# Optimization experiments

Hardware: AMD Instinct MI355X
Metric: run time of the kernel (lower is better)

Reference implementation:

```python
import jax, jax.numpy as jnp
import numpy as np

N, E = 10000, 320000
IN_DIM, OUT_DIM, HEADS = 256, 32, 8
HD = OUT_DIM * HEADS  # 256
EPS = 1e-16  # PyG softmax epsilon


def _make_conv_params(key, in_dim, heads, d):
    hd = heads * d
    ks = jax.random.split(key, 8)
    s = 0.02
    return {
        'Wq': jax.random.normal(ks[0], (in_dim, hd)) * s,
        'bq': jnp.zeros((hd,)),
        'Wk': jax.random.normal(ks[1], (in_dim, hd)) * s,
        'bk': jnp.zeros((hd,)),
        'Wv': jax.random.normal(ks[2], (in_dim, hd)) * s,
        'bv': jnp.zeros((hd,)),
        'We': jax.random.normal(ks[3], (1, hd)) * s,          # lin_edge, no bias
        'Wskip': jax.random.normal(ks[4], (in_dim, hd)) * s,  # lin_skip
        'bskip': jnp.zeros((hd,)),
        'Wbeta': jax.random.normal(ks[5], (3 * hd, 1)) * s,   # lin_beta, no bias
    }


def transformer_conv(x, src, dst, edge_attr, p, heads, d):
    # x: [N, F]; edge_attr: [E, 1]
    n = x.shape[0]
    q = (x @ p['Wq'] + p['bq']).reshape(n, heads, d)
    k = (x @ p['Wk'] + p['bk']).reshape(n, heads, d)
    v = (x @ p['Wv'] + p['bv']).reshape(n, heads, d)
    e = (edge_attr @ p['We']).reshape(-1, heads, d)  # [E, H, D]
    kj = k[src] + e                                  # [E, H, D]
    vj = v[src] + e
    # per-edge attention logits
    alpha = jnp.einsum('ehd,ehd->eh', q[dst], kj) / jnp.sqrt(jnp.asarray(d, x.dtype))
    # segment softmax over incoming edges of each dst node
    m = jax.ops.segment_max(alpha, dst, num_segments=n)     # [N, H]
    m = jnp.where(jnp.isfinite(m), m, 0.0)
    ex = jnp.exp(alpha - m[dst])
    denom = jax.ops.segment_sum(ex, dst, num_segments=n)    # [N, H]
    w = ex / (denom[dst] + EPS)                              # [E, H]
    out = jax.ops.segment_sum(w[:, :, None] * vj, dst, num_segments=n)  # [N, H, D]
    out = out.reshape(n, heads * d)
    # beta-gated skip connection
    xr = x @ p['Wskip'] + p['bskip']
    beta = jax.nn.sigmoid(jnp.concatenate([out, xr, out - xr], axis=-1) @ p['Wbeta'])  # [N, 1]
    return beta * xr + (1.0 - beta) * out


def setup_inputs() -> dict:
    key = jax.random.key(0)
    kx, ke, kw, k1, k2 = jax.random.split(key, 5)
    inp = {
        'x': jax.random.normal(kx, (N, IN_DIM), dtype=jnp.float32),
        'edge_index': jax.random.randint(ke, (2, E), 0, N, dtype=jnp.int64),
        'edge_weight': jax.random.uniform(kw, (E,), dtype=jnp.float32),
    }
    p1 = _make_conv_params(k1, IN_DIM, HEADS, OUT_DIM)
    p2 = _make_conv_params(k2, HD, HEADS, OUT_DIM)
    for name, v in p1.items():
        inp[name + '1'] = v
    for name, v in p2.items():
        inp[name + '2'] = v
    return inp


def reference(x, edge_index, edge_weight,
              Wq1, bq1, Wk1, bk1, Wv1, bv1, We1, Wskip1, bskip1, Wbeta1,
              Wq2, bq2, Wk2, bk2, Wv2, bv2, We2, Wskip2, bskip2, Wbeta2):
    src, dst = edge_index[0], edge_index[1]
    ea = edge_weight[:, None]  # [E, 1]
    p1 = dict(Wq=Wq1, bq=bq1, Wk=Wk1, bk=bk1, Wv=Wv1, bv=bv1, We=We1,
              Wskip=Wskip1, bskip=bskip1, Wbeta=Wbeta1)
    p2 = dict(Wq=Wq2, bq=bq2, Wk=Wk2, bk=bk2, Wv=Wv2, bv=bv2, We=We2,
              Wskip=Wskip2, bskip=bskip2, Wbeta=Wbeta2)
    h = transformer_conv(x, src, dst, ea, p1, HEADS, OUT_DIM)
    h = transformer_conv(h, src, dst, ea, p2, HEADS, OUT_DIM)
    h = transformer_conv(h, src, dst, ea, p2, HEADS, OUT_DIM)  # conv2 applied twice, shared weights
    return h
```

## Files before the change

### kernel.cpp

```cpp
#include <hip/hip_runtime.h>
#include <hip/hip_bf16.h>
#include <math.h>

#define NN 10000
#define EE 320000
#define DIM 256
#define NROWS 10016
#define SCANB 40

typedef __attribute__((ext_vector_type(8))) _Float16 f16x8;
typedef __attribute__((ext_vector_type(4))) _Float16 f16x4;
typedef __attribute__((ext_vector_type(4))) float f32x4;

__device__ __forceinline__ float bf2f(unsigned short u) {
  union { unsigned int ui; float f; } cv;
  cv.ui = ((unsigned int)u) << 16;
  return cv.f;
}

__global__ void k_detect(const unsigned int* __restrict__ xw, const int* __restrict__ ei,
                         int* __restrict__ flags) {
  int lane = threadIdx.x;
  int wild = 0;
  for (int t = 0; t < 16; ++t) {
    unsigned int w = xw[t * 64 + lane];
    unsigned int lo = w & 0xffffu;
    float f = bf2f((unsigned short)lo);
    float af = fabsf(f);
    if (lo != 0u && (af > 1e4f || af < 1e-30f)) wild++;
  }
  #pragma unroll
  for (int m = 1; m < 64; m <<= 1) wild += __shfl_xor(wild, m);
  int zeros = 0;
  for (int t = 0; t < 2; ++t) {
    if (ei[(t * 64 + lane) * 2 + 1] == 0) zeros++;
  }
  #pragma unroll
  for (int m = 1; m < 64; m <<= 1) zeros += __shfl_xor(zeros, m);
  if (lane == 0) {
    flags[0] = (wild > 100) ? 1 : 0;
    flags[1] = (zeros > 100) ? 1 : 0;
  }
}

struct PBatch { const void* src[20]; int off[21]; };

__global__ void k_cvt_params(PBatch b, float* __restrict__ out, const int* __restrict__ flags) {
  int isf = flags[0];
  int total = b.off[20];
  for (int i = blockIdx.x * blockDim.x + threadIdx.x; i < total; i += gridDim.x * blockDim.x) {
    int k = 0;
    while (i >= b.off[k + 1]) k++;
    int j = i - b.off[k];
    out[i] = isf ? ((const float*)b.src[k])[j] : bf2f(((const unsigned short*)b.src[k])[j]);
  }
}

__global__ void k_split_x(const void* __restrict__ in, _Float16* __restrict__ Ah,
                          _Float16* __restrict__ Al, const int* __restrict__ flags) {
  int isf = flags[0];
  int i = blockIdx.x * blockDim.x + threadIdx.x;
  if (i >= NROWS * DIM / 4) return;
  f16x4 h, l;
  if (i >= NN * DIM / 4) {
    h = (f16x4)(_Float16)0.f;
    l = (f16x4)(_Float16)0.f;
  } else {
    float v[4];
    if (isf) {
      float4 t = reinterpret_cast<const float4*>(in)[i];
      v[0] = t.x; v[1] = t.y; v[2] = t.z; v[3] = t.w;
    } else {
      ushort4 t = reinterpret_cast<const ushort4*>(in)[i];
      v[0] = bf2f(t.x); v[1] = bf2f(t.y); v[2] = bf2f(t.z); v[3] = bf2f(t.w);
    }
    #pragma unroll
    for (int j = 0; j < 4; ++j) {
      _Float16 hh = (_Float16)v[j];
      h[j] = hh;
      l[j] = (_Float16)(v[j] - (float)hh);
    }
  }
  reinterpret_cast<f16x4*>(Ah)[i] = h;
  reinterpret_cast<f16x4*>(Al)[i] = l;
}

struct WPtrs { const float* W[8]; };

__global__ void k_split_w(WPtrs wp, _Float16* __restrict__ Bh) {
  int i = blockIdx.x * blockDim.x + threadIdx.x;
  if (i >= 8 * 65536) return;
  int m = i >> 16;
  int col = (i >> 8) & 255;
  int k = i & 255;
  Bh[i] = (_Float16)wp.W[m][k * 256 + col];
}

struct BPtrs { const float* B[8]; };

__global__ void k_bias(BPtrs bp, float* __restrict__ bvec) {
  int i = blockIdx.x * blockDim.x + threadIdx.x;
  if (i >= 2048) return;
  int m = i >> 8;
  bvec[i] = bp.B[m][i & 255];
}

__global__ void k_idx_count(const int* __restrict__ ei, int* __restrict__ s32,
                            int* __restrict__ d32, int* __restrict__ counts,
                            const int* __restrict__ flags) {
  int i64 = flags[1];
  int i = blockIdx.x * blockDim.x + threadIdx.x;
  if (i < EE) {
    int s, d;
    if (i64) { s = ei[2 * i]; d = ei[2 * (EE + i)]; }
    else     { s = ei[i];     d = ei[EE + i]; }
    s32[i] = s; d32[i] = d;
    atomicAdd(&counts[d], 1);
  }
}

__global__ __launch_bounds__(256) void k_scan1(const int* __restrict__ counts,
                                               int* __restrict__ tmpoff,
                                               int* __restrict__ bsum) {
  __shared__ int s[256];
  int t = threadIdx.x;
  int i = blockIdx.x * 256 + t;
  int v = (i < NN) ? counts[i] : 0;
  s[t] = v;
  __syncthreads();
  for (int off = 1; off < 256; off <<= 1) {
    int x = (t >= off) ? s[t - off] : 0;
    __syncthreads();
    s[t] += x;
    __syncthreads();
  }
  if (i < NN) tmpoff[i] = s[t] - v;
  if (t == 255) bsum[blockIdx.x] = s[255];
}

__global__ void k_scan2(const int* __restrict__ bsum, int* __restrict__ bbase) {
  int lane = threadIdx.x;
  int v = (lane < SCANB) ? bsum[lane] : 0;
  int incl = v;
  #pragma unroll
  for (int off = 1; off < 64; off <<= 1) {
    int t = __shfl_up(incl, off);
    if (lane >= off) incl += t;
  }
  if (lane < SCANB) bbase[lane] = incl - v;
}

__global__ __launch_bounds__(256) void k_scan3(const int* __restrict__ tmpoff,
                                               const int* __restrict__ bbase,
                                               int* __restrict__ offsets,
                                               int* __restrict__ cursor) {
  int i = blockIdx.x * 256 + threadIdx.x;
  if (i < NN) {
    int o = tmpoff[i] + bbase[i >> 8];
    offsets[i] = o;
    cursor[i] = o;
  }
  if (i == 0) offsets[NN] = EE;
}

__global__ void k_fill_sort(const int* __restrict__ d32, const int* __restrict__ s32,
                            const void* __restrict__ ew, int* __restrict__ cursor,
                            int* __restrict__ srcS, float* __restrict__ wS,
                            const int* __restrict__ flags) {
  int isf = flags[0];
  int i = blockIdx.x * blockDim.x + threadIdx.x;
  if (i < EE) {
    float wv = isf ? ((const float*)ew)[i] : bf2f(((const unsigned short*)ew)[i]);
    int p = atomicAdd(&cursor[d32[i]], 1);
    srcS[p] = s32[i];
    wS[p] = wv;
  }
}

__global__ __launch_bounds__(256, 4) void k_gemm_mfma(
    const _Float16* __restrict__ Ah, const _Float16* __restrict__ Al,
    const _Float16* __restrict__ Bh, const float* __restrict__ bvec,
    float* __restrict__ Qf, _Float16* __restrict__ KVh, float* __restrict__ XRf) {
  int tid = (int)threadIdx.x;
  int wave = tid >> 6, lane = tid & 63;
  int lr = lane & 15;
  int kg = (lane >> 4) << 3;
  int mat = blockIdx.y;
  int rowBase = blockIdx.x << 5;
  int colBase = (mat << 8) + (wave << 6);
  const _Float16* a0 = Ah + (size_t)(rowBase + lr) * 256 + kg;
  const _Float16* a1 = Al + (size_t)(rowBase + lr) * 256 + kg;
  const _Float16* b0 = Bh + (size_t)(colBase + lr) * 256 + kg;
  f32x4 acc[2][4] = {};
  #pragma unroll
  for (int ks = 0; ks < 256; ks += 32) {
    f16x8 ah0 = *reinterpret_cast<const f16x8*>(a0 + ks);
    f16x8 ah1 = *reinterpret_cast<const f16x8*>(a0 + 16 * 256 + ks);
    f16x8 bh[4];
    #pragma unroll
    for (int cf = 0; cf < 4; ++cf)
      bh[cf] = *reinterpret_cast<const f16x8*>(b0 + cf * 16 * 256 + ks);
    #pragma unroll
    for (int cf = 0; cf < 4; ++cf) {
      acc[0][cf] = __builtin_amdgcn_mfma_f32_16x16x32_f16(ah0, bh[cf], acc[0][cf], 0, 0, 0);
      acc[1][cf] = __builtin_amdgcn_mfma_f32_16x16x32_f16(ah1, bh[cf], acc[1][cf], 0, 0, 0);
    }
    if (mat == 3) {
      f16x8 al0 = *reinterpret_cast<const f16x8*>(a1 + ks);
      f16x8 al1 = *reinterpret_cast<const f16x8*>(a1 + 16 * 256 + ks);
      #pragma unroll
      for (int cf = 0; cf < 4; ++cf) {
        acc[0][cf] = __builtin_amdgcn_mfma_f32_16x16x32_f16(al0, bh[cf], acc[0][cf], 0, 0, 0);
        acc[1][cf] = __builtin_amdgcn_mfma_f32_16x16x32_f16(al1, bh[cf], acc[1][cf], 0, 0, 0);
      }
    }
  }
  int rj = (lane >> 4) << 2;
  int colLoc = (wave << 6);
  #pragma unroll
  for (int rf = 0; rf < 2; ++rf) {
    #pragma unroll
    for (int cf = 0; cf < 4; ++cf) {
      int col = colLoc + cf * 16 + lr;
      float bb = bvec[(mat << 8) + col];
      #pragma unroll
      for (int j = 0; j < 4; ++j) {
        int row = rowBase + rf * 16 + rj + j;
        if (row < NN) {
          float val = acc[rf][cf][j] + bb;
          if (mat == 0)      Qf[(size_t)row * DIM + col] = val;
          else if (mat == 3) XRf[(size_t)row * DIM + col] = val;
          else KVh[(size_t)row * 512 + ((mat == 2) ? 256 : 0) + col] = (_Float16)val;
        }
      }
    }
  }
}

#define ATT_STEP(KK, VV, WW) do { \
    float part = q4.x * fmaf(WW, we4.x, (float)KK[0]) + q4.y * fmaf(WW, we4.y, (float)KK[1]) \
               + q4.z * fmaf(WW, we4.z, (float)KK[2]) + q4.w * fmaf(WW, we4.w, (float)KK[3]); \
    part += __shfl_xor(part, 1); \
    part += __shfl_xor(part, 2); \
    part += __shfl_xor(part, 4); \
    float alpha = part * 0.17677669529663687f; \
    float nm = fmaxf(m, alpha); \
    float sc = __expf(m - nm); \
    float pe = __expf(alpha - nm); \
    l = l * sc + pe; \
    a0 = fmaf(a0, sc, pe * fmaf(WW, we4.x, (float)VV[0])); \
    a1 = fmaf(a1, sc, pe * fmaf(WW, we4.y, (float)VV[1])); \
    a2 = fmaf(a2, sc, pe * fmaf(WW, we4.z, (float)VV[2])); \
    a3 = fmaf(a3, sc, pe * fmaf(WW, we4.w, (float)VV[3])); \
    m = nm; \
  } while (0)

__global__ __launch_bounds__(256) void k_attn(
    const float* __restrict__ Qf, const _Float16* __restrict__ KVh,
    const float* __restrict__ XRf, const float* __restrict__ We,
    const float* __restrict__ Wb, const int* __restrict__ srcS,
    const float* __restrict__ wS, const int* __restrict__ offsets,
    _Float16* __restrict__ Ah, _Float16* __restrict__ Al,
    float* __restrict__ FinalOut) {
  int wid = (int)threadIdx.x >> 6, lane = (int)threadIdx.x & 63;
  int node = blockIdx.x * 4 + wid;
  if (node >= NN) return;
  int d0 = lane * 4;
  const float4 q4 = *reinterpret_cast<const float4*>(&Qf[(size_t)node * DIM + d0]);
  const float4 x4 = *reinterpret_cast<const float4*>(&XRf[(size_t)node * DIM + d0]);
  const float4 we4 = *reinterpret_cast<const float4*>(&We[d0]);
  const float4 wo = *reinterpret_cast<const float4*>(&Wb[d0]);
  const float4 wx = *reinterpret_cast<const float4*>(&Wb[DIM + d0]);
  const float4 wd = *reinterpret_cast<const float4*>(&Wb[2 * DIM + d0]);
  int beg = offsets[node], end = offsets[node + 1];
  beg = __builtin_amdgcn_readfirstlane(beg);
  end = __builtin_amdgcn_readfirstlane(end);
  float m = -INFINITY, l = 0.f, a0 = 0.f, a1 = 0.f, a2 = 0.f, a3 = 0.f;
  if (end > beg) {
    int pLast = end - 1;
    int sA = srcS[beg];
    float wA = wS[beg];
    int p1 = (beg + 1 <= pLast) ? beg + 1 : pLast;
    int sB = srcS[p1];
    float wB = wS[p1];
    const _Float16* rA = KVh + (size_t)sA * 512 + d0;
    const _Float16* rB = KVh + (size_t)sB * 512 + d0;
    f16x4 kA = *reinterpret_cast<const f16x4*>(rA);
    f16x4 vA = *reinterpret_cast<const f16x4*>(rA + 256);
    f16x4 kB = *reinterpret_cast<const f16x4*>(rB);
    f16x4 vB = *reinterpret_cast<const f16x4*>(rB + 256);
    int p = beg;
    #pragma unroll 2
    for (; p + 2 < end; ++p) {
      int sN = srcS[p + 2];
      float wN = wS[p + 2];
      const _Float16* rN = KVh + (size_t)sN * 512 + d0;
      f16x4 kN = *reinterpret_cast<const f16x4*>(rN);
      f16x4 vN = *reinterpret_cast<const f16x4*>(rN + 256);
      ATT_STEP(kA, vA, wA);
      kA = kB; vA = vB; wA = wB;
      kB = kN; vB = vN; wB = wN;
    }
    ATT_STEP(kA, vA, wA);
    if (p + 1 < end) ATT_STEP(kB, vB, wB);
  }
  float inv = 1.f / (l + 1e-16f);
  float o0 = a0 * inv, o1 = a1 * inv, o2 = a2 * inv, o3 = a3 * inv;
  float part = o0 * wo.x + o1 * wo.y + o2 * wo.z + o3 * wo.w
             + x4.x * wx.x + x4.y * wx.y + x4.z * wx.z + x4.w * wx.w
             + (o0 - x4.x) * wd.x + (o1 - x4.y) * wd.y
             + (o2 - x4.z) * wd.z + (o3 - x4.w) * wd.w;
  #pragma unroll
  for (int msk = 1; msk < 64; msk <<= 1) part += __shfl_xor(part, msk);
  float beta = 1.f / (1.f + __expf(-part));
  float h0 = beta * x4.x + (1.f - beta) * o0;
  float h1 = beta * x4.y + (1.f - beta) * o1;
  float h2 = beta * x4.z + (1.f - beta) * o2;
  float h3 = beta * x4.w + (1.f - beta) * o3;
  if (FinalOut) {
    float4 h; h.x = h0; h.y = h1; h.z = h2; h.w = h3;
    *reinterpret_cast<float4*>(&FinalOut[(size_t)node * DIM + d0]) = h;
  } else {
    f16x4 hh, ll;
    _Float16 t0 = (_Float16)h0, t1 = (_Float16)h1, t2 = (_Float16)h2, t3 = (_Float16)h3;
    hh[0] = t0; hh[1] = t1; hh[2] = t2; hh[3] = t3;
    ll[0] = (_Float16)(h0 - (float)t0); ll[1] = (_Float16)(h1 - (float)t1);
    ll[2] = (_Float16)(h2 - (float)t2); ll[3] = (_Float16)(h3 - (float)t3);
    *reinterpret_cast<f16x4*>(&Ah[(size_t)node * DIM + d0]) = hh;
    *reinterpret_cast<f16x4*>(&Al[(size_t)node * DIM + d0]) = ll;
  }
}

static inline size_t align256(size_t v) { return (v + 255) & ~(size_t)255; }

extern "C" void kernel_launch(void* const* d_in, const int* in_sizes, int n_in,
                              void* d_out, int out_size, void* d_ws, size_t ws_size,
                              hipStream_t stream) {
  const void* x = d_in[0];
  const int* eidx = (const int*)d_in[1];
  const void* ew = d_in[2];

  char* w = (char*)d_ws;
  size_t pos = 0;
  int* flags = (int*)(w + pos); pos = align256(pos + 2 * sizeof(int));
  float* Qf  = (float*)(w + pos); pos = align256(pos + (size_t)NROWS * DIM * 4);
  float* XRf = (float*)(w + pos); pos = align256(pos + (size_t)NROWS * DIM * 4);
  _Float16* KVh = (_Float16*)(w + pos); pos = align256(pos + (size_t)NROWS * 512 * 2);
  _Float16* Ah = (_Float16*)(w + pos); pos = align256(pos + (size_t)NROWS * DIM * 2);
  _Float16* Al = (_Float16*)(w + pos); pos = align256(pos + (size_t)NROWS * DIM * 2);
  _Float16* Bh = (_Float16*)(w + pos); pos = align256(pos + (size_t)8 * 65536 * 2);
  float* bvec = (float*)(w + pos);  pos = align256(pos + 2048 * 4);
  int* s32   = (int*)(w + pos);    pos = align256(pos + (size_t)EE * 4);
  int* d32   = (int*)(w + pos);    pos = align256(pos + (size_t)EE * 4);
  int* srcS  = (int*)(w + pos);    pos = align256(pos + (size_t)EE * 4);
  float* wS  = (float*)(w + pos);  pos = align256(pos + (size_t)EE * 4);
  int* counts  = (int*)(w + pos);  pos = align256(pos + (size_t)NN * 4);
  int* offsets = (int*)(w + pos);  pos = align256(pos + (size_t)(NN + 1) * 4);
  int* cursor  = (int*)(w + pos);  pos = align256(pos + (size_t)NN * 4);
  int* tmpoff  = (int*)(w + pos);  pos = align256(pos + (size_t)NN * 4);
  int* bsum    = (int*)(w + pos);  pos = align256(pos + 64 * 4);
  int* bbase   = (int*)(w + pos);  pos = align256(pos + 64 * 4);
  float* Pf    = (float*)(w + pos);

  PBatch pb;
  int off = 0;
  for (int i = 0; i < 20; ++i) {
    pb.src[i] = d_in[3 + i];
    pb.off[i] = off;
    off += in_sizes[3 + i];
  }
  pb.off[20] = off;

  k_detect<<<1, 64, 0, stream>>>((const unsigned int*)x, eidx, flags);
  hipMemsetAsync(counts, 0, (size_t)NN * 4, stream);
  k_idx_count<<<(EE + 255) / 256, 256, 0, stream>>>(eidx, s32, d32, counts, flags);
  k_scan1<<<SCANB, 256, 0, stream>>>(counts, tmpoff, bsum);
  k_scan2<<<1, 64, 0, stream>>>(bsum, bbase);
  k_scan3<<<SCANB, 256, 0, stream>>>(tmpoff, bbase, offsets, cursor);
  k_fill_sort<<<(EE + 255) / 256, 256, 0, stream>>>(d32, s32, ew, cursor, srcS, wS, flags);
  k_cvt_params<<<2064, 256, 0, stream>>>(pb, Pf, flags);

  const float* P[20];
  for (int i = 0; i < 20; ++i) P[i] = Pf + pb.off[i];

  WPtrs wp;
  BPtrs bp;
  for (int g = 0; g < 2; ++g) {
    const float* const* pp = &P[g * 10];
    wp.W[g * 4 + 0] = pp[0]; wp.W[g * 4 + 1] = pp[2];
    wp.W[g * 4 + 2] = pp[4]; wp.W[g * 4 + 3] = pp[7];
    bp.B[g * 4 + 0] = pp[1]; bp.B[g * 4 + 1] = pp[3];
    bp.B[g * 4 + 2] = pp[5]; bp.B[g * 4 + 3] = pp[8];
  }
  k_split_w<<<(8 * 65536 + 255) / 256, 256, 0, stream>>>(wp, Bh);
  k_bias<<<8, 256, 0, stream>>>(bp, bvec);
  k_split_x<<<(NROWS * DIM / 4 + 255) / 256, 256, 0, stream>>>(x, Ah, Al, flags);

  for (int layer = 0; layer < 3; ++layer) {
    int g = (layer == 0) ? 0 : 1;
    const float* const* pp = &P[g * 10];
    k_gemm_mfma<<<dim3(NROWS / 32, 4), 256, 0, stream>>>(
        Ah, Al, Bh + (size_t)g * 4 * 65536, bvec + g * 1024, Qf, KVh, XRf);
    k_attn<<<(NN + 3) / 4, 256, 0, stream>>>(Qf, KVh, XRf, pp[6], pp[9],
        srcS, wS, offsets, Ah, Al, (layer == 2) ? (float*)d_out : nullptr);
  }
}
```

Baseline: 331.2 us.

## Fuse setup kernels, pack edge src/weight, process attention edges in pairs

Merges parameter conversion, weight transpose, bias copy, and x split into one pack kernel, folds the counts memset into the detect kernel, and removes the separate block-scan kernel by having each scan3 block sum preceding block totals. Sorted edges now store source index and weight interleaved as int2, so one load fetches both. The attention loop handles two edges per step with a shared max/rescale and prefetches two pairs ahead. This cuts launch count and per-edge exp/rescale work, at the cost of higher register pressure in the attention kernel.

```diff
diff --git a/kernel.cpp b/kernel.cpp
--- a/kernel.cpp
+++ b/kernel.cpp
@@ -18,91 +18,39 @@
   return cv.f;
 }
 
-__global__ void k_detect(const unsigned int* __restrict__ xw, const int* __restrict__ ei,
-                         int* __restrict__ flags) {
-  int lane = threadIdx.x;
-  int wild = 0;
-  for (int t = 0; t < 16; ++t) {
-    unsigned int w = xw[t * 64 + lane];
-    unsigned int lo = w & 0xffffu;
-    float f = bf2f((unsigned short)lo);
-    float af = fabsf(f);
-    if (lo != 0u && (af > 1e4f || af < 1e-30f)) wild++;
-  }
-  #pragma unroll
-  for (int m = 1; m < 64; m <<= 1) wild += __shfl_xor(wild, m);
-  int zeros = 0;
-  for (int t = 0; t < 2; ++t) {
-    if (ei[(t * 64 + lane) * 2 + 1] == 0) zeros++;
-  }
-  #pragma unroll
-  for (int m = 1; m < 64; m <<= 1) zeros += __shfl_xor(zeros, m);
-  if (lane == 0) {
-    flags[0] = (wild > 100) ? 1 : 0;
-    flags[1] = (zeros > 100) ? 1 : 0;
-  }
-}
-
-struct PBatch { const void* src[20]; int off[21]; };
-
-__global__ void k_cvt_params(PBatch b, float* __restrict__ out, const int* __restrict__ flags) {
-  int isf = flags[0];
-  int total = b.off[20];
-  for (int i = blockIdx.x * blockDim.x + threadIdx.x; i < total; i += gridDim.x * blockDim.x) {
-    int k = 0;
-    while (i >= b.off[k + 1]) k++;
-    int j = i - b.off[k];
-    out[i] = isf ? ((const float*)b.src[k])[j] : bf2f(((const unsigned short*)b.src[k])[j]);
-  }
-}
-
-__global__ void k_split_x(const void* __restrict__ in, _Float16* __restrict__ Ah,
-                          _Float16* __restrict__ Al, const int* __restrict__ flags) {
-  int isf = flags[0];
-  int i = blockIdx.x * blockDim.x + threadIdx.x;
-  if (i >= NROWS * DIM / 4) return;
-  f16x4 h, l;
-  if (i >= NN * DIM / 4) {
-    h = (f16x4)(_Float16)0.f;
-    l = (f16x4)(_Float16)0.f;
-  } else {
-    float v[4];
-    if (isf) {
-      float4 t = reinterpret_cast<const float4*>(in)[i];
-      v[0] = t.x; v[1] = t.y; v[2] = t.z; v[3] = t.w;
-    } else {
-      ushort4 t = reinterpret_cast<const ushort4*>(in)[i];
-      v[0] = bf2f(t.x); v[1] = bf2f(t.y); v[2] = bf2f(t.z); v[3] = bf2f(t.w);
-    }
-    #pragma unroll
-    for (int j = 0; j < 4; ++j) {
-      _Float16 hh = (_Float16)v[j];
-      h[j] = hh;
-      l[j] = (_Float16)(v[j] - (float)hh);
-    }
-  }
-  reinterpret_cast<f16x4*>(Ah)[i] = h;
-  reinterpret_cast<f16x4*>(Al)[i] = l;
-}
-
-struct WPtrs { const float* W[8]; };
-
-__global__ void k_split_w(WPtrs wp, _Float16* __restrict__ Bh) {
-  int i = blockIdx.x * blockDim.x + threadIdx.x;
-  if (i >= 8 * 65536) return;
-  int m = i >> 16;
-  int col = (i >> 8) & 255;
-  int k = i & 255;
-  Bh[i] = (_Float16)wp.W[m][k * 256 + col];
-}
-
-struct BPtrs { const float* B[8]; };
-
-__global__ void k_bias(BPtrs bp, float* __restrict__ bvec) {
-  int i = blockIdx.x * blockDim.x + threadIdx.x;
-  if (i >= 2048) return;
-  int m = i >> 8;
-  bvec[i] = bp.B[m][i & 255];
+__device__ __forceinline__ float ldf(const void* p, int idx, int isf) {
+  return isf ? ((const float*)p)[idx] : bf2f(((const unsigned short*)p)[idx]);
+}
+
+__global__ __launch_bounds__(256) void k_detect_zero(const unsigned int* __restrict__ xw,
+                                                     const int* __restrict__ ei,
+                                                     int* __restrict__ flags,
+                                                     int* __restrict__ counts) {
+  int i = blockIdx.x * 256 + (int)threadIdx.x;
+  if (i < NN) counts[i] = 0;
+  if (blockIdx.x == 0 && threadIdx.x < 64) {
+    int lane = threadIdx.x;
+    int wild = 0;
+    for (int t = 0; t < 16; ++t) {
+      unsigned int w = xw[t * 64 + lane];
+      unsigned int lo = w & 0xffffu;
+      float f = bf2f((unsigned short)lo);
+      float af = fabsf(f);
+      if (lo != 0u && (af > 1e4f || af < 1e-30f)) wild++;
+    }
+    #pragma unroll
+    for (int m = 1; m < 64; m <<= 1) wild += __shfl_xor(wild, m);
+    int zeros = 0;
+    for (int t = 0; t < 2; ++t) {
+      if (ei[(t * 64 + lane) * 2 + 1] == 0) zeros++;
+    }
+    #pragma unroll
+    for (int m = 1; m < 64; m <<= 1) zeros += __shfl_xor(zeros, m);
+    if (lane == 0) {
+      flags[0] = (wild > 100) ? 1 : 0;
+      flags[1] = (zeros > 100) ? 1 : 0;
+    }
+  }
 }
 
 __global__ void k_idx_count(const int* __restrict__ ei, int* __restrict__ s32,
@@ -138,25 +86,23 @@
   if (t == 255) bsum[blockIdx.x] = s[255];
 }
 
-__global__ void k_scan2(const int* __restrict__ bsum, int* __restrict__ bbase) {
-  int lane = threadIdx.x;
-  int v = (lane < SCANB) ? bsum[lane] : 0;
-  int incl = v;
-  #pragma unroll
-  for (int off = 1; off < 64; off <<= 1) {
-    int t = __shfl_up(incl, off);
-    if (lane >= off) incl += t;
-  }
-  if (lane < SCANB) bbase[lane] = incl - v;
-}
-
 __global__ __launch_bounds__(256) void k_scan3(const int* __restrict__ tmpoff,
-                                               const int* __restrict__ bbase,
+                                               const int* __restrict__ bsum,
                                                int* __restrict__ offsets,
                                                int* __restrict__ cursor) {
-  int i = blockIdx.x * 256 + threadIdx.x;
+  __shared__ int sbase;
+  if (threadIdx.x < 64) {
+    int t = threadIdx.x;
+    int v = (t < SCANB && t < (int)blockIdx.x) ? bsum[t] : 0;
+    #pragma unroll
+    for (int msk = 1; msk < 64; msk <<= 1) v += __shfl_xor(v, msk);
+    if (t == 0) sbase = v;
+  }
+  __syncthreads();
+  int base = sbase;
+  int i = blockIdx.x * 256 + (int)threadIdx.x;
   if (i < NN) {
-    int o = tmpoff[i] + bbase[i >> 8];
+    int o = tmpoff[i] + base;
     offsets[i] = o;
     cursor[i] = o;
   }
@@ -165,15 +111,75 @@
 
 __global__ void k_fill_sort(const int* __restrict__ d32, const int* __restrict__ s32,
                             const void* __restrict__ ew, int* __restrict__ cursor,
-                            int* __restrict__ srcS, float* __restrict__ wS,
-                            const int* __restrict__ flags) {
+                            int2* __restrict__ eS, const int* __restrict__ flags) {
   int isf = flags[0];
   int i = blockIdx.x * blockDim.x + threadIdx.x;
   if (i < EE) {
     float wv = isf ? ((const float*)ew)[i] : bf2f(((const unsigned short*)ew)[i]);
     int p = atomicAdd(&cursor[d32[i]], 1);
-    srcS[p] = s32[i];
-    wS[p] = wv;
+    eS[p] = make_int2(s32[i], __float_as_int(wv));
+  }
+}
+
+struct PackArgs {
+  const void* W[8];
+  const void* B8[8];
+  const void* WeWb[4];
+  const void* x;
+};
+
+__global__ __launch_bounds__(256) void k_pack(PackArgs pa, _Float16* __restrict__ Bh,
+                                              float* __restrict__ bvec,
+                                              float* __restrict__ WeWbF,
+                                              _Float16* __restrict__ Ah,
+                                              _Float16* __restrict__ Al,
+                                              const int* __restrict__ flags) {
+  int isf = flags[0];
+  int i = blockIdx.x * 256 + (int)threadIdx.x;
+  if (i < 8 * 65536) {
+    int m = i >> 16, col = (i >> 8) & 255, k = i & 255;
+    Bh[i] = (_Float16)ldf(pa.W[m], k * 256 + col, isf);
+    return;
+  }
+  i -= 8 * 65536;
+  if (i < 2048) {
+    bvec[i] = ldf(pa.B8[i >> 8], i & 255, isf);
+    return;
+  }
+  i -= 2048;
+  if (i < 2048) {
+    int which, k;
+    if (i < 256)       { which = 0; k = i; }
+    else if (i < 1024) { which = 1; k = i - 256; }
+    else if (i < 1280) { which = 2; k = i - 1024; }
+    else               { which = 3; k = i - 1280; }
+    WeWbF[i] = ldf(pa.WeWb[which], k, isf);
+    return;
+  }
+  i -= 2048;
+  if (i < NROWS * 64) {
+    f16x4 h, l;
+    if (i >= NN * 64) {
+      h = (f16x4)(_Float16)0.f;
+      l = (f16x4)(_Float16)0.f;
+    } else {
+      float v[4];
+      if (isf) {
+        float4 t = reinterpret_cast<const float4*>(pa.x)[i];
+        v[0] = t.x; v[1] = t.y; v[2] = t.z; v[3] = t.w;
+      } else {
+        ushort4 t = reinterpret_cast<const ushort4*>(pa.x)[i];
+        v[0] = bf2f(t.x); v[1] = bf2f(t.y); v[2] = bf2f(t.z); v[3] = bf2f(t.w);
+      }
+      #pragma unroll
+      for (int j = 0; j < 4; ++j) {
+        _Float16 hh = (_Float16)v[j];
+        h[j] = hh;
+        l[j] = (_Float16)(v[j] - (float)hh);
+      }
+    }
+    reinterpret_cast<f16x4*>(Ah)[i] = h;
+    reinterpret_cast<f16x4*>(Al)[i] = l;
   }
 }
 
@@ -247,7 +253,7 @@
     float nm = fmaxf(m, alpha); \
     float sc = __expf(m - nm); \
     float pe = __expf(alpha - nm); \
-    l = l * sc + pe; \
+    l = fmaf(l, sc, pe); \
     a0 = fmaf(a0, sc, pe * fmaf(WW, we4.x, (float)VV[0])); \
     a1 = fmaf(a1, sc, pe * fmaf(WW, we4.y, (float)VV[1])); \
     a2 = fmaf(a2, sc, pe * fmaf(WW, we4.z, (float)VV[2])); \
@@ -255,13 +261,34 @@
     m = nm; \
   } while (0)
 
+#define PAIR_STEP(K0, V0, W0, K1, V1, W1) do { \
+    float pt0 = q4.x * fmaf(W0, we4.x, (float)K0[0]) + q4.y * fmaf(W0, we4.y, (float)K0[1]) \
+              + q4.z * fmaf(W0, we4.z, (float)K0[2]) + q4.w * fmaf(W0, we4.w, (float)K0[3]); \
+    float pt1 = q4.x * fmaf(W1, we4.x, (float)K1[0]) + q4.y * fmaf(W1, we4.y, (float)K1[1]) \
+              + q4.z * fmaf(W1, we4.z, (float)K1[2]) + q4.w * fmaf(W1, we4.w, (float)K1[3]); \
+    pt0 += __shfl_xor(pt0, 1); pt1 += __shfl_xor(pt1, 1); \
+    pt0 += __shfl_xor(pt0, 2); pt1 += __shfl_xor(pt1, 2); \
+    pt0 += __shfl_xor(pt0, 4); pt1 += __shfl_xor(pt1, 4); \
+    float al0 = pt0 * 0.17677669529663687f; \
+    float al1 = pt1 * 0.17677669529663687f; \
+    float nm = fmaxf(fmaxf(m, al0), al1); \
+    float sc = __expf(m - nm); \
+    float p0 = __expf(al0 - nm); \
+    float p1 = __expf(al1 - nm); \
+    l = fmaf(l, sc, p0 + p1); \
+    a0 = fmaf(a0, sc, fmaf(p0, fmaf(W0, we4.x, (float)V0[0]), p1 * fmaf(W1, we4.x, (float)V1[0]))); \
+    a1 = fmaf(a1, sc, fmaf(p0, fmaf(W0, we4.y, (float)V0[1]), p1 * fmaf(W1, we4.y, (float)V1[1]))); \
+    a2 = fmaf(a2, sc, fmaf(p0, fmaf(W0, we4.z, (float)V0[2]), p1 * fmaf(W1, we4.z, (float)V1[2]))); \
+    a3 = fmaf(a3, sc, fmaf(p0, fmaf(W0, we4.w, (float)V0[3]), p1 * fmaf(W1, we4.w, (float)V1[3]))); \
+    m = nm; \
+  } while (0)
+
 __global__ __launch_bounds__(256) void k_attn(
     const float* __restrict__ Qf, const _Float16* __restrict__ KVh,
     const float* __restrict__ XRf, const float* __restrict__ We,
-    const float* __restrict__ Wb, const int* __restrict__ srcS,
-    const float* __restrict__ wS, const int* __restrict__ offsets,
-    _Float16* __restrict__ Ah, _Float16* __restrict__ Al,
-    float* __restrict__ FinalOut) {
+    const float* __restrict__ Wb, const int2* __restrict__ eS,
+    const int* __restrict__ offsets, _Float16* __restrict__ Ah,
+    _Float16* __restrict__ Al, float* __restrict__ FinalOut) {
   int wid = (int)threadIdx.x >> 6, lane = (int)threadIdx.x & 63;
   int node = blockIdx.x * 4 + wid;
   if (node >= NN) return;
@@ -276,33 +303,44 @@
   beg = __builtin_amdgcn_readfirstlane(beg);
   end = __builtin_amdgcn_readfirstlane(end);
   float m = -INFINITY, l = 0.f, a0 = 0.f, a1 = 0.f, a2 = 0.f, a3 = 0.f;
-  if (end > beg) {
-    int pLast = end - 1;
-    int sA = srcS[beg];
-    float wA = wS[beg];
-    int p1 = (beg + 1 <= pLast) ? beg + 1 : pLast;
-    int sB = srcS[p1];
-    float wB = wS[p1];
-    const _Float16* rA = KVh + (size_t)sA * 512 + d0;
-    const _Float16* rB = KVh + (size_t)sB * 512 + d0;
-    f16x4 kA = *reinterpret_cast<const f16x4*>(rA);
-    f16x4 vA = *reinterpret_cast<const f16x4*>(rA + 256);
-    f16x4 kB = *reinterpret_cast<const f16x4*>(rB);
-    f16x4 vB = *reinterpret_cast<const f16x4*>(rB + 256);
-    int p = beg;
+  int p = beg;
+  if ((end - beg) & 1) {
+    int2 e = eS[p];
+    float w0 = __int_as_float(e.y);
+    const _Float16* r = KVh + (size_t)e.x * 512 + d0;
+    f16x4 k0 = *reinterpret_cast<const f16x4*>(r);
+    f16x4 v0 = *reinterpret_cast<const f16x4*>(r + 256);
+    ATT_STEP(k0, v0, w0);
+    ++p;
+  }
+  if (p < end) {
+    int2 eA0 = eS[p], eA1 = eS[p + 1];
+    int pb = (p + 3 < end) ? (p + 2) : p;
+    int2 eB0 = eS[pb], eB1 = eS[pb + 1];
+    const _Float16* rA0 = KVh + (size_t)eA0.x * 512 + d0;
+    const _Float16* rA1 = KVh + (size_t)eA1.x * 512 + d0;
+    const _Float16* rB0 = KVh + (size_t)eB0.x * 512 + d0;
+    const _Float16* rB1 = KVh + (size_t)eB1.x * 512 + d0;
+    f16x4 kA0 = *reinterpret_cast<const f16x4*>(rA0), vA0 = *reinterpret_cast<const f16x4*>(rA0 + 256);
+    f16x4 kA1 = *reinterpret_cast<const f16x4*>(rA1), vA1 = *reinterpret_cast<const f16x4*>(rA1 + 256);
+    f16x4 kB0 = *reinterpret_cast<const f16x4*>(rB0), vB0 = *reinterpret_cast<const f16x4*>(rB0 + 256);
+    f16x4 kB1 = *reinterpret_cast<const f16x4*>(rB1), vB1 = *reinterpret_cast<const f16x4*>(rB1 + 256);
+    float wA0 = __int_as_float(eA0.y), wA1 = __int_as_float(eA1.y);
+    float wB0 = __int_as_float(eB0.y), wB1 = __int_as_float(eB1.y);
     #pragma unroll 2
-    for (; p + 2 < end; ++p) {
-      int sN = srcS[p + 2];
-      float wN = wS[p + 2];
-      const _Float16* rN = KVh + (size_t)sN * 512 + d0;
-      f16x4 kN = *reinterpret_cast<const f16x4*>(rN);
-      f16x4 vN = *reinterpret_cast<const f16x4*>(rN + 256);
-      ATT_STEP(kA, vA, wA);
-      kA = kB; vA = vB; wA = wB;
-      kB = kN; vB = vN; wB = wN;
-    }
-    ATT_STEP(kA, vA, wA);
-    if (p + 1 < end) ATT_STEP(kB, vB, wB);
+    for (; p + 2 < end; p += 2) {
+      int pc = (p + 5 < end) ? (p + 4) : p;
+      int2 eC0 = eS[pc], eC1 = eS[pc + 1];
+      const _Float16* rC0 = KVh + (size_t)eC0.x * 512 + d0;
+      const _Float16* rC1 = KVh + (size_t)eC1.x * 512 + d0;
+      f16x4 kC0 = *reinterpret_cast<const f16x4*>(rC0), vC0 = *reinterpret_cast<const f16x4*>(rC0 + 256);
+      f16x4 kC1 = *reinterpret_cast<const f16x4*>(rC1), vC1 = *reinterpret_cast<const f16x4*>(rC1 + 256);
+      float wC0 = __int_as_float(eC0.y), wC1 = __int_as_float(eC1.y);
+      PAIR_STEP(kA0, vA0, wA0, kA1, vA1, wA1);
+      kA0 = kB0; vA0 = vB0; wA0 = wB0; kA1 = kB1; vA1 = vB1; wA1 = wB1;
+      kB0 = kC0; vB0 = vC0; wB0 = wC0; kB1 = kC1; vB1 = vC1; wB1 = wC1;
+    }
+    PAIR_STEP(kA0, vA0, wA0, kA1, vA1, wA1);
   }
   float inv = 1.f / (l + 1e-16f);
   float o0 = a0 * inv, o1 = a1 * inv, o2 = a2 * inv, o3 = a3 * inv;
@@ -349,59 +387,42 @@
   _Float16* Ah = (_Float16*)(w + pos); pos = align256(pos + (size_t)NROWS * DIM * 2);
   _Float16* Al = (_Float16*)(w + pos); pos = align256(pos + (size_t)NROWS * DIM * 2);
   _Float16* Bh = (_Float16*)(w + pos); pos = align256(pos + (size_t)8 * 65536 * 2);
-  float* bvec = (float*)(w + pos);  pos = align256(pos + 2048 * 4);
+  float* bvec  = (float*)(w + pos); pos = align256(pos + 2048 * 4);
+  float* WeWbF = (float*)(w + pos); pos = align256(pos + 2048 * 4);
   int* s32   = (int*)(w + pos);    pos = align256(pos + (size_t)EE * 4);
   int* d32   = (int*)(w + pos);    pos = align256(pos + (size_t)EE * 4);
-  int* srcS  = (int*)(w + pos);    pos = align256(pos + (size_t)EE * 4);
-  float* wS  = (float*)(w + pos);  pos = align256(pos + (size_t)EE * 4);
+  int2* eS   = (int2*)(w + pos);   pos = align256(pos + (size_t)EE * 8);
   int* counts  = (int*)(w + pos);  pos = align256(pos + (size_t)NN * 4);
   int* offsets = (int*)(w + pos);  pos = align256(pos + (size_t)(NN + 1) * 4);
   int* cursor  = (int*)(w + pos);  pos = align256(pos + (size_t)NN * 4);
   int* tmpoff  = (int*)(w + pos);  pos = align256(pos + (size_t)NN * 4);
   int* bsum    = (int*)(w + pos);  pos = align256(pos + 64 * 4);
-  int* bbase   = (int*)(w + pos);  pos = align256(pos + 64 * 4);
-  float* Pf    = (float*)(w + pos);
-
-  PBatch pb;
-  int off = 0;
-  for (int i = 0; i < 20; ++i) {
-    pb.src[i] = d_in[3 + i];
-    pb.off[i] = off;
-    off += in_sizes[3 + i];
-  }
-  pb.off[20] = off;
-
-  k_detect<<<1, 64, 0, stream>>>((const unsigned int*)x, eidx, flags);
-  hipMemsetAsync(counts, 0, (size_t)NN * 4, stream);
+
+  PackArgs pa;
+  pa.x = x;
+  for (int g = 0; g < 2; ++g) {
+    const void* const* pp = &d_in[3 + g * 10];
+    pa.W[g * 4 + 0] = pp[0]; pa.W[g * 4 + 1] = pp[2];
+    pa.W[g * 4 + 2] = pp[4]; pa.W[g * 4 + 3] = pp[7];
+    pa.B8[g * 4 + 0] = pp[1]; pa.B8[g * 4 + 1] = pp[3];
+    pa.B8[g * 4 + 2] = pp[5]; pa.B8[g * 4 + 3] = pp[8];
+    pa.WeWb[g * 2 + 0] = pp[6];
+    pa.WeWb[g * 2 + 1] = pp[9];
+  }
+
+  k_detect_zero<<<SCANB, 256, 0, stream>>>((const unsigned int*)x, eidx, flags, counts);
+  k_pack<<<4568, 256, 0, stream>>>(pa, Bh, bvec, WeWbF, Ah, Al, flags);
   k_idx_count<<<(EE + 255) / 256, 256, 0, stream>>>(eidx, s32, d32, counts, flags);
   k_scan1<<<SCANB, 256, 0, stream>>>(counts, tmpoff, bsum);
-  k_scan2<<<1, 64, 0, stream>>>(bsum, bbase);
-  k_scan3<<<SCANB, 256, 0, stream>>>(tmpoff, bbase, offsets, cursor);
-  k_fill_sort<<<(EE + 255) / 256, 256, 0, stream>>>(d32, s32, ew, cursor, srcS, wS, flags);
-  k_cvt_params<<<2064, 256, 0, stream>>>(pb, Pf, flags);
-
-  const float* P[20];
-  for (int i = 0; i < 20; ++i) P[i] = Pf + pb.off[i];
-
-  WPtrs wp;
-  BPtrs bp;
-  for (int g = 0; g < 2; ++g) {
-    const float* const* pp = &P[g * 10];
-    wp.W[g * 4 + 0] = pp[0]; wp.W[g * 4 + 1] = pp[2];
-    wp.W[g * 4 + 2] = pp[4]; wp.W[g * 4 + 3] = pp[7];
-    bp.B[g * 4 + 0] = pp[1]; bp.B[g * 4 + 1] = pp[3];
-    bp.B[g * 4 + 2] = pp[5]; bp.B[g * 4 + 3] = pp[8];
-  }
-  k_split_w<<<(8 * 65536 + 255) / 256, 256, 0, stream>>>(wp, Bh);
-  k_bias<<<8, 256, 0, stream>>>(bp, bvec);
-  k_split_x<<<(NROWS * DIM / 4 + 255) / 256, 256, 0, stream>>>(x, Ah, Al, flags);
+  k_scan3<<<SCANB, 256, 0, stream>>>(tmpoff, bsum, offsets, cursor);
+  k_fill_sort<<<(EE + 255) / 256, 256, 0, stream>>>(d32, s32, ew, cursor, eS, flags);
 
   for (int layer = 0; layer < 3; ++layer) {
     int g = (layer == 0) ? 0 : 1;
-    const float* const* pp = &P[g * 10];
     k_gemm_mfma<<<dim3(NROWS / 32, 4), 256, 0, stream>>>(
         Ah, Al, Bh + (size_t)g * 4 * 65536, bvec + g * 1024, Qf, KVh, XRf);
-    k_attn<<<(NN + 3) / 4, 256, 0, stream>>>(Qf, KVh, XRf, pp[6], pp[9],
-        srcS, wS, offsets, Ah, Al, (layer == 2) ? (float*)d_out : nullptr);
-  }
-}
+    k_attn<<<(NN + 3) / 4, 256, 0, stream>>>(Qf, KVh, XRf,
+        WeWbF + (g ? 1024 : 0), WeWbF + (g ? 1280 : 256),
+        eS, offsets, Ah, Al, (layer == 2) ? (float*)d_out : nullptr);
+  }
+}
```

Result: faster. 308.4 us (-6.9%).
